# Optimization experiments

Hardware: AMD Instinct MI355X
Metric: run time of the kernel (lower is better)

Reference implementation:

```python
import jax, jax.numpy as jnp
import numpy as np

B, A, K, M = 8, 100000, 80, 32
ALPHA, GAMMA = 0.25, 2.0


def _make_boxes(rng, n, img=800.0):
    cx = rng.uniform(0, img, n).astype(np.float32)
    cy = rng.uniform(0, img, n).astype(np.float32)
    w = rng.uniform(16, 256, n).astype(np.float32)
    h = rng.uniform(16, 256, n).astype(np.float32)
    return np.stack([cx - w / 2, cy - h / 2, cx + w / 2, cy + h / 2], axis=1)


def setup_inputs() -> dict:
    key = jax.random.key(0)
    k1, k2 = jax.random.split(key)
    rng = np.random.default_rng(0)
    classifications = jax.random.uniform(k1, (B, A, K), dtype=jnp.float32)  # forward clamps to (1e-4, 1-1e-4)
    regressions = jax.random.normal(k2, (B, A, 4), dtype=jnp.float32)
    anchors = jnp.asarray(_make_boxes(rng, A))[None]  # [1, A, 4]
    boxes = _make_boxes(rng, B * M).reshape(B, M, 4)
    labels = rng.integers(0, K, (B, M)).astype(np.float32)
    labels[:, M * 3 // 4:] = -1.0  # padded (invalid) annotations
    annotations = jnp.asarray(np.concatenate([boxes, labels[..., None]], axis=-1))  # [B, M, 5]
    return {"classifications": classifications, "regressions": regressions,
            "anchors": anchors, "annotations": annotations}


def _calc_iou(a, b):
    # a: [A,4] anchors, b: [M,4] gt boxes (xyxy)
    area = (b[:, 2] - b[:, 0]) * (b[:, 3] - b[:, 1])  # [M]
    iw = jnp.clip(jnp.minimum(a[:, 2:3], b[None, :, 2]) - jnp.maximum(a[:, 0:1], b[None, :, 0]), 0)
    ih = jnp.clip(jnp.minimum(a[:, 3:4], b[None, :, 3]) - jnp.maximum(a[:, 1:2], b[None, :, 1]), 0)
    inter = iw * ih  # [A,M]
    ua = ((a[:, 2] - a[:, 0]) * (a[:, 3] - a[:, 1]))[:, None] + area[None] - inter
    return inter / jnp.clip(ua, 1e-8)


def _per_image(classification, regression, anchor, ann):
    label = ann[:, 4]
    valid = label != -1.0
    has_ann = jnp.any(valid)

    iou = _calc_iou(anchor, ann[:, :4])           # [A,M]
    iou = jnp.where(valid[None, :], iou, -1.0)    # mask padded annotations
    iou_max = jnp.max(iou, axis=1)                # [A]
    iou_argmax = jnp.argmax(iou, axis=1)
    assigned = ann[iou_argmax]                    # [A,5]

    positive = iou_max >= 0.5
    num_pos = jnp.sum(positive.astype(jnp.float32))
    one_hot = jax.nn.one_hot(assigned[:, 4].astype(jnp.int32), K, dtype=jnp.float32)  # [A,K]

    targets = jnp.where((iou_max >= 0.4)[:, None], 0.25, -1.0)
    targets = jnp.where(positive[:, None], one_hot, targets)  # 0 for pos anchors, 1 at assigned class

    # focal loss (detectron form)
    logit = jnp.clip(classification, 1e-4, 1.0 - 1e-4)
    p = jax.nn.sigmoid(logit)
    term1 = (1.0 - p) ** GAMMA * jnp.log(p)
    term2 = -(p ** GAMMA) * jnp.where(logit >= 0.0,
                                      logit + jax.nn.softplus(-logit),
                                      jax.nn.softplus(logit))
    cls_loss = -jnp.where(targets != 0.0, ALPHA * term1, (1.0 - ALPHA) * term2)
    cls_total = jnp.sum(cls_loss) / jnp.maximum(num_pos, 0.01)

    aw = anchor[:, 2] - anchor[:, 0]
    ah = anchor[:, 3] - anchor[:, 1]
    acx = anchor[:, 0] + 0.5 * aw
    acy = anchor[:, 1] + 0.5 * ah
    gw = assigned[:, 2] - assigned[:, 0]
    gh = assigned[:, 3] - assigned[:, 1]
    gcx = assigned[:, 0] + 0.5 * gw
    gcy = assigned[:, 1] + 0.5 * gh
    gw = jnp.clip(gw, 1.0)
    gh = jnp.clip(gh, 1.0)
    t = jnp.stack([(gcx - acx) / aw, (gcy - acy) / ah,
                   jnp.log(gw / aw), jnp.log(gh / ah)], axis=1)
    t = t / jnp.array([0.1, 0.1, 0.2, 0.2], dtype=jnp.float32)
    diff = jnp.abs(t - regression)
    sl1 = jnp.where(diff <= 1.0 / 9.0, 0.5 * 9.0 * diff * diff, diff - 0.5 / 9.0)
    reg_sum = jnp.sum(jnp.where(positive[:, None], sl1, 0.0))
    reg_loss = jnp.where(num_pos > 0, reg_sum / jnp.maximum(num_pos * 4.0, 1.0), 0.0)

    cls_total = jnp.where(has_ann, cls_total, 0.0)
    reg_loss = jnp.where(has_ann, reg_loss, 0.0)
    return cls_total, reg_loss


def reference(classifications, regressions, anchors, annotations):
    cls_l, reg_l = jax.vmap(_per_image, in_axes=(0, 0, None, 0))(
        classifications, regressions, anchors[0], annotations)
    return (jnp.mean(cls_l, keepdims=True), jnp.mean(reg_l, keepdims=True))
```

## Files before the change

kernel.cpp:

```cpp
#include <hip/hip_runtime.h>

#define BB 8
#define AA 100000
#define KK 80
#define MM 32
#define TILE 128
#define NBLK 782
#define NBLK_P 784

__device__ __forceinline__ float cls_term(float c, int code, int k) {
    float x   = __builtin_amdgcn_fmed3f(c, 1e-4f, 1.0f - 1e-4f);
    float em  = __expf(-x);
    float u   = 1.0f + em;
    float s   = __logf(u);
    float p   = __builtin_amdgcn_rcpf(u);
    float omp = 1.0f - p;
    bool use2 = (code >= 0) && (k != code);
    return use2 ? (0.75f * p * p * (x + s)) : (0.25f * omp * omp * s);
}

__device__ __forceinline__ float neg_term(float c) {
    float x   = __builtin_amdgcn_fmed3f(c, 1e-4f, 1.0f - 1e-4f);
    float em  = __expf(-x);
    float u   = 1.0f + em;
    float s   = __logf(u);
    float p   = __builtin_amdgcn_rcpf(u);
    float omp = 1.0f - p;
    return 0.25f * omp * omp * s;
}

__global__ __launch_bounds__(256)
void focal_main(const float* __restrict__ cls,
                const float* __restrict__ reg,
                const float* __restrict__ anc,
                const float* __restrict__ ann,
                float* __restrict__ cls_part,
                float* __restrict__ reg_part_g,
                int*   __restrict__ np_part)
{
    const int blk = blockIdx.x;
    const int b   = blockIdx.y;
    const int t   = threadIdx.x;
    const int a0  = blk * TILE;
    const int nA  = min(TILE, AA - a0);
    const bool full = (nA == TILE);

    __shared__ float s_ann[MM * 5];
    __shared__ int   s_code[TILE];
    __shared__ float s_wred[4];
    __shared__ int   s_wnp[4];
    __shared__ float s_wrg[4];

    float annv = 0.0f;
    if (t < MM * 5) annv = ann[b * MM * 5 + t];
    const int ai = a0 + t;
    float4 av = make_float4(0.f, 0.f, 0.f, 0.f);
    if (t < nA) av = ((const float4*)anc)[ai];

    if (t < MM * 5) s_ann[t] = annv;
    __syncthreads();

    const float4* c4 = (const float4*)(cls + ((size_t)b * AA + (size_t)a0) * KK);
    float4 v[10];
    if (full) {
        #pragma unroll
        for (int j = 0; j < 10; ++j) v[j] = c4[j * 256 + t];
    }

    int   code     = -1;
    float reg_part = 0.0f;
    int   pos      = 0;
    if (t < nA) {
        const float ax1 = av.x, ay1 = av.y, ax2 = av.z, ay2 = av.w;
        float best = -2.0f;
        int   bidx = 0;
        const float a_area = (ax2 - ax1) * (ay2 - ay1);
        #pragma unroll
        for (int m = 0; m < MM; ++m) {
            float bx1 = s_ann[m * 5 + 0], by1 = s_ann[m * 5 + 1];
            float bx2 = s_ann[m * 5 + 2], by2 = s_ann[m * 5 + 3];
            float lab = s_ann[m * 5 + 4];
            float area  = (bx2 - bx1) * (by2 - by1);
            float iw    = fmaxf(fminf(ax2, bx2) - fmaxf(ax1, bx1), 0.0f);
            float ih    = fmaxf(fminf(ay2, by2) - fmaxf(ay1, by1), 0.0f);
            float inter = iw * ih;
            float ua    = fmaxf(a_area + area - inter, 1e-8f);
            float iou   = inter / ua;
            if (lab == -1.0f) iou = -1.0f;
            if (iou > best) { best = iou; bidx = m; }
        }
        if (best >= 0.5f) {
            pos  = 1;
            code = (int)s_ann[bidx * 5 + 4];
            float gx1 = s_ann[bidx * 5 + 0], gy1 = s_ann[bidx * 5 + 1];
            float gx2 = s_ann[bidx * 5 + 2], gy2 = s_ann[bidx * 5 + 3];
            float aw  = ax2 - ax1,  ah  = ay2 - ay1;
            float acx = ax1 + 0.5f * aw, acy = ay1 + 0.5f * ah;
            float gw  = gx2 - gx1,  gh  = gy2 - gy1;
            float gcx = gx1 + 0.5f * gw, gcy = gy1 + 0.5f * gh;
            gw = fmaxf(gw, 1.0f); gh = fmaxf(gh, 1.0f);
            float tt0 = ((gcx - acx) / aw) / 0.1f;
            float tt1 = ((gcy - acy) / ah) / 0.1f;
            float tt2 = logf(gw / aw) / 0.2f;
            float tt3 = logf(gh / ah) / 0.2f;
            const float4 rv = ((const float4*)reg)[(size_t)b * AA + ai];
            float d0 = fabsf(tt0 - rv.x);
            float d1 = fabsf(tt1 - rv.y);
            float d2 = fabsf(tt2 - rv.z);
            float d3 = fabsf(tt3 - rv.w);
            const float th = 1.0f / 9.0f, hb = 0.5f / 9.0f;
            reg_part  = (d0 <= th ? 4.5f * d0 * d0 : d0 - hb)
                      + (d1 <= th ? 4.5f * d1 * d1 : d1 - hb)
                      + (d2 <= th ? 4.5f * d2 * d2 : d2 - hb)
                      + (d3 <= th ? 4.5f * d3 * d3 : d3 - hb);
        }
    }
    if (t < TILE) s_code[t] = code;

    {
        unsigned long long bal = __ballot(pos != 0);
        int wnp = __popcll(bal);
        float wrg = reg_part;
        #pragma unroll
        for (int off = 32; off > 0; off >>= 1) wrg += __shfl_down(wrg, off, 64);
        int wid  = t >> 6;
        int lane = t & 63;
        if (lane == 0) { s_wnp[wid] = wnp; s_wrg[wid] = wrg; }
    }
    __syncthreads();
    if (t == 0) {
        int   np = s_wnp[0] + s_wnp[1] + s_wnp[2] + s_wnp[3];
        float rg = s_wrg[0] + s_wrg[1] + s_wrg[2] + s_wrg[3];
        np_part   [b * NBLK_P + blk] = np;
        reg_part_g[b * NBLK_P + blk] = rg;
    }

    float part = 0.0f;
    auto process = [&](const float4 vv, int idx4) {
        unsigned e  = (unsigned)idx4 * 4u;
        unsigned al = e / 80u;
        unsigned k0 = e - al * 80u;
        int ca = s_code[al];
        if (__ballot(ca >= 0) == 0ULL) {
            part += neg_term(vv.x);
            part += neg_term(vv.y);
            part += neg_term(vv.z);
            part += neg_term(vv.w);
        } else {
            part += cls_term(vv.x, ca, (int)k0);
            part += cls_term(vv.y, ca, (int)k0 + 1);
            part += cls_term(vv.z, ca, (int)k0 + 2);
            part += cls_term(vv.w, ca, (int)k0 + 3);
        }
    };

    if (full) {
        #pragma unroll
        for (int j = 0; j < 10; ++j) process(v[j], j * 256 + t);
    } else {
        const int limit4 = nA * (KK / 4);
        #pragma unroll 4
        for (int j = 0; j < 10; ++j) {
            int idx4 = j * 256 + t;
            if (idx4 < limit4) { float4 vv = c4[idx4]; process(vv, idx4); }
        }
    }

    #pragma unroll
    for (int off = 32; off > 0; off >>= 1) part += __shfl_down(part, off, 64);
    if ((t & 63) == 0) s_wred[t >> 6] = part;
    __syncthreads();
    if (t == 0) {
        float tot = s_wred[0] + s_wred[1] + s_wred[2] + s_wred[3];
        cls_part[b * NBLK_P + blk] = tot;
    }
}

__global__ __launch_bounds__(256)
void focal_final(const float* __restrict__ ann,
                 const float* __restrict__ cls_part,
                 const float* __restrict__ reg_part,
                 const int*   __restrict__ np_part,
                 float* __restrict__ out)
{
    const int t    = threadIdx.x;
    const int lane = t & 63, wid = t >> 6;
    __shared__ double sd[4];
    __shared__ float  sf[4];
    __shared__ int    si[4];
    __shared__ float  s_c[BB], s_r[BB];

    for (int b = 0; b < BB; ++b) {
        double cd = 0.0; float rf = 0.0f; int np = 0;
        for (int j = t; j < NBLK; j += 256) {
            cd += (double)cls_part[b * NBLK_P + j];
            rf += reg_part[b * NBLK_P + j];
            np += np_part [b * NBLK_P + j];
        }
        #pragma unroll
        for (int off = 32; off > 0; off >>= 1) {
            cd += __shfl_down(cd, off, 64);
            rf += __shfl_down(rf, off, 64);
            np += __shfl_down(np, off, 64);
        }
        if (lane == 0) { sd[wid] = cd; sf[wid] = rf; si[wid] = np; }
        __syncthreads();
        if (t == 0) {
            double cdt = sd[0] + sd[1] + sd[2] + sd[3];
            float  rft = sf[0] + sf[1] + sf[2] + sf[3];
            int    npt = si[0] + si[1] + si[2] + si[3];
            bool has = false;
            for (int m = 0; m < MM; ++m)
                has |= (ann[b * MM * 5 + m * 5 + 4] != -1.0f);
            float npf  = (float)npt;
            float ctot = (float)cdt / fmaxf(npf, 0.01f);
            float rtot = (npt > 0) ? (rft / fmaxf(npf * 4.0f, 1.0f)) : 0.0f;
            s_c[b] = has ? ctot : 0.0f;
            s_r[b] = has ? rtot : 0.0f;
        }
        __syncthreads();
    }
    if (t == 0) {
        float c = 0.0f, r = 0.0f;
        for (int b = 0; b < BB; ++b) { c += s_c[b]; r += s_r[b]; }
        out[0] = c / (float)BB;
        out[1] = r / (float)BB;
    }
}

extern "C" void kernel_launch(void* const* d_in, const int* in_sizes, int n_in,
                              void* d_out, int out_size, void* d_ws, size_t ws_size,
                              hipStream_t stream) {
    const float* cls = (const float*)d_in[0];
    const float* reg = (const float*)d_in[1];
    const float* anc = (const float*)d_in[2];
    const float* ann = (const float*)d_in[3];
    float* out = (float*)d_out;

    float* cls_part = (float*)d_ws;
    float* reg_part = cls_part + BB * NBLK_P;
    int*   np_part  = (int*)(reg_part + BB * NBLK_P);

    dim3 grid(NBLK, BB);
    focal_main<<<grid, 256, 0, stream>>>(cls, reg, anc, ann,
                                         cls_part, reg_part, np_part);
    focal_final<<<1, 256, 0, stream>>>(ann, cls_part, reg_part, np_part, out);
}
```

Baseline: 379.4 us.

## Split anchor matching and classification loss into separate kernels with grid-stride streaming

Splits the fused kernel in two. The first computes each anchor's IoU assignment, regression loss and positive count, and writes a per-anchor class code to workspace. The second streams the classification tensor with a fixed 256-block-per-image grid, batching 8 float4 loads per thread per step and reading codes from global memory. The goal is to stop the IoU loop from sitting between the large classification loads and the math, and to fix occupancy with launch bounds. The cost is an extra launch plus a write and re-read of the codes array (about 3.2 MB).

```diff
diff --git a/kernel.cpp b/kernel.cpp
--- a/kernel.cpp
+++ b/kernel.cpp
@@ -4,9 +4,11 @@
 #define AA 100000
 #define KK 80
 #define MM 32
-#define TILE 128
-#define NBLK 782
-#define NBLK_P 784
+#define NB1 391
+#define NB1_P 392
+#define K2BLK 256
+#define K2STRIDE (K2BLK * 256)
+#define TOTAL4 (AA * KK / 4)
 
 __device__ __forceinline__ float cls_term(float c, int code, int k) {
     float x   = __builtin_amdgcn_fmed3f(c, 1e-4f, 1.0f - 1e-4f);
@@ -30,47 +32,31 @@
 }
 
 __global__ __launch_bounds__(256)
-void focal_main(const float* __restrict__ cls,
-                const float* __restrict__ reg,
-                const float* __restrict__ anc,
-                const float* __restrict__ ann,
-                float* __restrict__ cls_part,
-                float* __restrict__ reg_part_g,
-                int*   __restrict__ np_part)
+void focal_anchors(const float* __restrict__ reg,
+                   const float* __restrict__ anc,
+                   const float* __restrict__ ann,
+                   int*   __restrict__ codes,
+                   float* __restrict__ reg_part_g,
+                   int*   __restrict__ np_part)
 {
     const int blk = blockIdx.x;
     const int b   = blockIdx.y;
     const int t   = threadIdx.x;
-    const int a0  = blk * TILE;
-    const int nA  = min(TILE, AA - a0);
-    const bool full = (nA == TILE);
+    const int a   = blk * 256 + t;
+    const bool act = (a < AA);
 
     __shared__ float s_ann[MM * 5];
-    __shared__ int   s_code[TILE];
-    __shared__ float s_wred[4];
     __shared__ int   s_wnp[4];
     __shared__ float s_wrg[4];
 
-    float annv = 0.0f;
-    if (t < MM * 5) annv = ann[b * MM * 5 + t];
-    const int ai = a0 + t;
-    float4 av = make_float4(0.f, 0.f, 0.f, 0.f);
-    if (t < nA) av = ((const float4*)anc)[ai];
-
-    if (t < MM * 5) s_ann[t] = annv;
+    if (t < MM * 5) s_ann[t] = ann[b * MM * 5 + t];
     __syncthreads();
-
-    const float4* c4 = (const float4*)(cls + ((size_t)b * AA + (size_t)a0) * KK);
-    float4 v[10];
-    if (full) {
-        #pragma unroll
-        for (int j = 0; j < 10; ++j) v[j] = c4[j * 256 + t];
-    }
 
     int   code     = -1;
     float reg_part = 0.0f;
     int   pos      = 0;
-    if (t < nA) {
+    if (act) {
+        const float4 av = ((const float4*)anc)[a];
         const float ax1 = av.x, ay1 = av.y, ax2 = av.z, ay2 = av.w;
         float best = -2.0f;
         int   bidx = 0;
@@ -103,7 +89,7 @@
             float tt1 = ((gcy - acy) / ah) / 0.1f;
             float tt2 = logf(gw / aw) / 0.2f;
             float tt3 = logf(gh / ah) / 0.2f;
-            const float4 rv = ((const float4*)reg)[(size_t)b * AA + ai];
+            const float4 rv = ((const float4*)reg)[(size_t)b * AA + a];
             float d0 = fabsf(tt0 - rv.x);
             float d1 = fabsf(tt1 - rv.y);
             float d2 = fabsf(tt2 - rv.z);
@@ -115,7 +101,7 @@
                       + (d3 <= th ? 4.5f * d3 * d3 : d3 - hb);
         }
     }
-    if (t < TILE) s_code[t] = code;
+    if (act) codes[b * AA + a] = code;
 
     {
         unsigned long long bal = __ballot(pos != 0);
@@ -123,24 +109,32 @@
         float wrg = reg_part;
         #pragma unroll
         for (int off = 32; off > 0; off >>= 1) wrg += __shfl_down(wrg, off, 64);
-        int wid  = t >> 6;
-        int lane = t & 63;
-        if (lane == 0) { s_wnp[wid] = wnp; s_wrg[wid] = wrg; }
+        if ((t & 63) == 0) { s_wnp[t >> 6] = wnp; s_wrg[t >> 6] = wrg; }
     }
     __syncthreads();
     if (t == 0) {
-        int   np = s_wnp[0] + s_wnp[1] + s_wnp[2] + s_wnp[3];
-        float rg = s_wrg[0] + s_wrg[1] + s_wrg[2] + s_wrg[3];
-        np_part   [b * NBLK_P + blk] = np;
-        reg_part_g[b * NBLK_P + blk] = rg;
-    }
+        np_part   [b * NB1_P + blk] = s_wnp[0] + s_wnp[1] + s_wnp[2] + s_wnp[3];
+        reg_part_g[b * NB1_P + blk] = s_wrg[0] + s_wrg[1] + s_wrg[2] + s_wrg[3];
+    }
+}
+
+__global__ __launch_bounds__(256, 8)
+void focal_cls(const float* __restrict__ cls,
+               const int*   __restrict__ codes,
+               float* __restrict__ cls_part)
+{
+    const int b   = blockIdx.y;
+    const int t   = threadIdx.x;
+    const int gid = blockIdx.x * 256 + t;
+    const float4* __restrict__ c4  = (const float4*)(cls + (size_t)b * ((size_t)AA * KK));
+    const int*    __restrict__ cod = codes + b * AA;
 
     float part = 0.0f;
-    auto process = [&](const float4 vv, int idx4) {
-        unsigned e  = (unsigned)idx4 * 4u;
-        unsigned al = e / 80u;
-        unsigned k0 = e - al * 80u;
-        int ca = s_code[al];
+
+    auto process = [&](const float4 vv, int g) {
+        unsigned q  = (unsigned)g / 20u;
+        unsigned k0 = ((unsigned)g - q * 20u) * 4u;
+        int ca = cod[q];
         if (__ballot(ca >= 0) == 0ULL) {
             part += neg_term(vv.x);
             part += neg_term(vv.y);
@@ -154,26 +148,37 @@
         }
     };
 
-    if (full) {
-        #pragma unroll
-        for (int j = 0; j < 10; ++j) process(v[j], j * 256 + t);
-    } else {
-        const int limit4 = nA * (KK / 4);
-        #pragma unroll 4
-        for (int j = 0; j < 10; ++j) {
-            int idx4 = j * 256 + t;
-            if (idx4 < limit4) { float4 vv = c4[idx4]; process(vv, idx4); }
-        }
-    }
-
+    #pragma unroll 1
+    for (int sc = 0; sc < 3; ++sc) {
+        const int g0 = gid + sc * 8 * K2STRIDE;
+        float4 v[8];
+        #pragma unroll
+        for (int j = 0; j < 8; ++j) v[j] = c4[g0 + j * K2STRIDE];
+        #pragma unroll
+        for (int j = 0; j < 8; ++j) process(v[j], g0 + j * K2STRIDE);
+    }
+    {
+        const int g0 = gid + 24 * K2STRIDE;
+        float4 v[7];
+        #pragma unroll
+        for (int j = 0; j < 7; ++j) {
+            int g = g0 + j * K2STRIDE;
+            if (g < TOTAL4) v[j] = c4[g];
+        }
+        #pragma unroll
+        for (int j = 0; j < 7; ++j) {
+            int g = g0 + j * K2STRIDE;
+            if (g < TOTAL4) process(v[j], g);
+        }
+    }
+
+    __shared__ float s_wred[4];
     #pragma unroll
     for (int off = 32; off > 0; off >>= 1) part += __shfl_down(part, off, 64);
     if ((t & 63) == 0) s_wred[t >> 6] = part;
     __syncthreads();
-    if (t == 0) {
-        float tot = s_wred[0] + s_wred[1] + s_wred[2] + s_wred[3];
-        cls_part[b * NBLK_P + blk] = tot;
-    }
+    if (t == 0)
+        cls_part[b * K2BLK + blockIdx.x] = s_wred[0] + s_wred[1] + s_wred[2] + s_wred[3];
 }
 
 __global__ __launch_bounds__(256)
@@ -191,11 +196,11 @@
     __shared__ float  s_c[BB], s_r[BB];
 
     for (int b = 0; b < BB; ++b) {
-        double cd = 0.0; float rf = 0.0f; int np = 0;
-        for (int j = t; j < NBLK; j += 256) {
-            cd += (double)cls_part[b * NBLK_P + j];
-            rf += reg_part[b * NBLK_P + j];
-            np += np_part [b * NBLK_P + j];
+        double cd = (double)cls_part[b * K2BLK + t];
+        float rf = 0.0f; int np = 0;
+        for (int j = t; j < NB1; j += 256) {
+            rf += reg_part[b * NB1_P + j];
+            np += np_part [b * NB1_P + j];
         }
         #pragma unroll
         for (int off = 32; off > 0; off >>= 1) {
@@ -237,12 +242,16 @@
     const float* ann = (const float*)d_in[3];
     float* out = (float*)d_out;
 
-    float* cls_part = (float*)d_ws;
-    float* reg_part = cls_part + BB * NBLK_P;
-    int*   np_part  = (int*)(reg_part + BB * NBLK_P);
-
-    dim3 grid(NBLK, BB);
-    focal_main<<<grid, 256, 0, stream>>>(cls, reg, anc, ann,
-                                         cls_part, reg_part, np_part);
+    int*   codes    = (int*)d_ws;
+    float* cls_part = (float*)(codes + (size_t)BB * AA);
+    float* reg_part = cls_part + BB * K2BLK;
+    int*   np_part  = (int*)(reg_part + BB * NB1_P);
+
+    dim3 g1(NB1, BB);
+    focal_anchors<<<g1, 256, 0, stream>>>(reg, anc, ann, codes, reg_part, np_part);
+
+    dim3 g2(K2BLK, BB);
+    focal_cls<<<g2, 256, 0, stream>>>(cls, codes, cls_part);
+
     focal_final<<<1, 256, 0, stream>>>(ann, cls_part, reg_part, np_part, out);
 }
```

New measurement: 399.3 us. 1.05x slower.

## Split focal loss into polynomial negative term plus sparse positive-row correction

Applied to the files above, without the earlier changes.

Every element's negative focal term is now computed with a degree-12 Chebyshev-derived polynomial instead of exp/log/rcp. Positive anchors get a per-row correction, found by ballot and evaluated a whole wave at a time. The grid shrinks to 256 blocks per image, each striding through a flat float4 index space with double-buffered loads and two anchor rounds per thread, which also simplifies the final reduction. The polynomial approximation risks accuracy differences, and the correction pass adds scattered row reads for positives.

```diff
diff --git a/kernel.cpp b/kernel.cpp
--- a/kernel.cpp
+++ b/kernel.cpp
@@ -1,178 +1,180 @@
 #include <hip/hip_runtime.h>
+#include <cmath>
 
 #define BB 8
 #define AA 100000
 #define KK 80
 #define MM 32
-#define TILE 128
-#define NBLK 782
-#define NBLK_P 784
-
-__device__ __forceinline__ float cls_term(float c, int code, int k) {
+#define APB 391
+#define NXB 256
+#define ST4 (NXB * 256)
+#define TOTAL4 (AA * KK / 4)
+
+struct FPoly {
+    float ih, nmid;
+    float a[13];
+};
+
+__device__ __forceinline__ float corr_term(float c, int ca, int k) {
     float x   = __builtin_amdgcn_fmed3f(c, 1e-4f, 1.0f - 1e-4f);
     float em  = __expf(-x);
     float u   = 1.0f + em;
     float s   = __logf(u);
     float p   = __builtin_amdgcn_rcpf(u);
     float omp = 1.0f - p;
-    bool use2 = (code >= 0) && (k != code);
-    return use2 ? (0.75f * p * p * (x + s)) : (0.25f * omp * omp * s);
-}
-
-__device__ __forceinline__ float neg_term(float c) {
-    float x   = __builtin_amdgcn_fmed3f(c, 1e-4f, 1.0f - 1e-4f);
-    float em  = __expf(-x);
-    float u   = 1.0f + em;
-    float s   = __logf(u);
-    float p   = __builtin_amdgcn_rcpf(u);
-    float omp = 1.0f - p;
-    return 0.25f * omp * omp * s;
-}
-
-__global__ __launch_bounds__(256)
+    float t2  = 0.75f * p * p * (x + s);
+    float t1  = 0.25f * omp * omp * s;
+    return (k == ca) ? 0.0f : (t2 - t1);
+}
+
+__device__ __forceinline__ float pneg(float c, const FPoly& P) {
+    float x  = __builtin_amdgcn_fmed3f(c, 1e-4f, 1.0f - 1e-4f);
+    float tt = __builtin_fmaf(x, P.ih, P.nmid);
+    float r  = P.a[12];
+    #pragma unroll
+    for (int k = 11; k >= 0; --k) r = __builtin_fmaf(r, tt, P.a[k]);
+    return r;
+}
+
+__global__ __launch_bounds__(256, 4)
 void focal_main(const float* __restrict__ cls,
                 const float* __restrict__ reg,
                 const float* __restrict__ anc,
                 const float* __restrict__ ann,
+                FPoly P,
                 float* __restrict__ cls_part,
                 float* __restrict__ reg_part_g,
                 int*   __restrict__ np_part)
 {
-    const int blk = blockIdx.x;
-    const int b   = blockIdx.y;
-    const int t   = threadIdx.x;
-    const int a0  = blk * TILE;
-    const int nA  = min(TILE, AA - a0);
-    const bool full = (nA == TILE);
+    const int blk = blockIdx.x, b = blockIdx.y, t = threadIdx.x;
+    const int gid = blk * 256 + t;
+    const float*  __restrict__ cbase = cls + (size_t)b * ((size_t)AA * KK);
+    const float4* __restrict__ c4    = (const float4*)cbase;
 
     __shared__ float s_ann[MM * 5];
-    __shared__ int   s_code[TILE];
-    __shared__ float s_wred[4];
-    __shared__ int   s_wnp[4];
-    __shared__ float s_wrg[4];
-
-    float annv = 0.0f;
-    if (t < MM * 5) annv = ann[b * MM * 5 + t];
-    const int ai = a0 + t;
-    float4 av = make_float4(0.f, 0.f, 0.f, 0.f);
-    if (t < nA) av = ((const float4*)anc)[ai];
-
-    if (t < MM * 5) s_ann[t] = annv;
+    __shared__ float s_wc[4];
+    __shared__ float s_wr[4];
+    __shared__ int   s_wn[4];
+
+    if (t < MM * 5) s_ann[t] = ann[b * MM * 5 + t];
     __syncthreads();
 
-    const float4* c4 = (const float4*)(cls + ((size_t)b * AA + (size_t)a0) * KK);
-    float4 v[10];
-    if (full) {
-        #pragma unroll
-        for (int j = 0; j < 10; ++j) v[j] = c4[j * 256 + t];
-    }
-
-    int   code     = -1;
-    float reg_part = 0.0f;
-    int   pos      = 0;
-    if (t < nA) {
-        const float ax1 = av.x, ay1 = av.y, ax2 = av.z, ay2 = av.w;
-        float best = -2.0f;
-        int   bidx = 0;
-        const float a_area = (ax2 - ax1) * (ay2 - ay1);
-        #pragma unroll
-        for (int m = 0; m < MM; ++m) {
-            float bx1 = s_ann[m * 5 + 0], by1 = s_ann[m * 5 + 1];
-            float bx2 = s_ann[m * 5 + 2], by2 = s_ann[m * 5 + 3];
-            float lab = s_ann[m * 5 + 4];
-            float area  = (bx2 - bx1) * (by2 - by1);
-            float iw    = fmaxf(fminf(ax2, bx2) - fmaxf(ax1, bx1), 0.0f);
-            float ih    = fmaxf(fminf(ay2, by2) - fmaxf(ay1, by1), 0.0f);
-            float inter = iw * ih;
-            float ua    = fmaxf(a_area + area - inter, 1e-8f);
-            float iou   = inter / ua;
-            if (lab == -1.0f) iou = -1.0f;
-            if (iou > best) { best = iou; bidx = m; }
-        }
-        if (best >= 0.5f) {
-            pos  = 1;
-            code = (int)s_ann[bidx * 5 + 4];
-            float gx1 = s_ann[bidx * 5 + 0], gy1 = s_ann[bidx * 5 + 1];
-            float gx2 = s_ann[bidx * 5 + 2], gy2 = s_ann[bidx * 5 + 3];
-            float aw  = ax2 - ax1,  ah  = ay2 - ay1;
-            float acx = ax1 + 0.5f * aw, acy = ay1 + 0.5f * ah;
-            float gw  = gx2 - gx1,  gh  = gy2 - gy1;
-            float gcx = gx1 + 0.5f * gw, gcy = gy1 + 0.5f * gh;
-            gw = fmaxf(gw, 1.0f); gh = fmaxf(gh, 1.0f);
-            float tt0 = ((gcx - acx) / aw) / 0.1f;
-            float tt1 = ((gcy - acy) / ah) / 0.1f;
-            float tt2 = logf(gw / aw) / 0.2f;
-            float tt3 = logf(gh / ah) / 0.2f;
-            const float4 rv = ((const float4*)reg)[(size_t)b * AA + ai];
-            float d0 = fabsf(tt0 - rv.x);
-            float d1 = fabsf(tt1 - rv.y);
-            float d2 = fabsf(tt2 - rv.z);
-            float d3 = fabsf(tt3 - rv.w);
-            const float th = 1.0f / 9.0f, hb = 0.5f / 9.0f;
-            reg_part  = (d0 <= th ? 4.5f * d0 * d0 : d0 - hb)
-                      + (d1 <= th ? 4.5f * d1 * d1 : d1 - hb)
-                      + (d2 <= th ? 4.5f * d2 * d2 : d2 - hb)
-                      + (d3 <= th ? 4.5f * d3 * d3 : d3 - hb);
-        }
-    }
-    if (t < TILE) s_code[t] = code;
-
-    {
+    const int a0  = blk * APB;
+    const int nAb = min(APB, AA - a0);
+
+    float4 av0 = make_float4(0.f, 0.f, 0.f, 0.f);
+    float4 av1 = make_float4(0.f, 0.f, 0.f, 0.f);
+    if (t < nAb)       av0 = ((const float4*)anc)[a0 + t];
+    if (256 + t < nAb) av1 = ((const float4*)anc)[a0 + 256 + t];
+
+    float4 vA[8], vB[8];
+    #pragma unroll
+    for (int j = 0; j < 8; ++j) vA[j] = c4[gid + j * ST4];
+
+    int np = 0; float rg = 0.f, corr = 0.f;
+    auto do_round = [&](int idx, const float4 av, int roundBase) {
+        int   code = -1; float rp = 0.f; int pos = 0;
+        if (idx < nAb) {
+            const int a = a0 + idx;
+            const float ax1 = av.x, ay1 = av.y, ax2 = av.z, ay2 = av.w;
+            float best = -2.0f;
+            int   bidx = 0;
+            const float a_area = (ax2 - ax1) * (ay2 - ay1);
+            #pragma unroll
+            for (int m = 0; m < MM; ++m) {
+                float bx1 = s_ann[m * 5 + 0], by1 = s_ann[m * 5 + 1];
+                float bx2 = s_ann[m * 5 + 2], by2 = s_ann[m * 5 + 3];
+                float lab = s_ann[m * 5 + 4];
+                float area  = (bx2 - bx1) * (by2 - by1);
+                float iw    = fmaxf(fminf(ax2, bx2) - fmaxf(ax1, bx1), 0.0f);
+                float ih    = fmaxf(fminf(ay2, by2) - fmaxf(ay1, by1), 0.0f);
+                float inter = iw * ih;
+                float ua    = fmaxf(a_area + area - inter, 1e-8f);
+                float iou   = inter / ua;
+                if (lab == -1.0f) iou = -1.0f;
+                if (iou > best) { best = iou; bidx = m; }
+            }
+            if (best >= 0.5f) {
+                pos  = 1;
+                code = (int)s_ann[bidx * 5 + 4];
+                float gx1 = s_ann[bidx * 5 + 0], gy1 = s_ann[bidx * 5 + 1];
+                float gx2 = s_ann[bidx * 5 + 2], gy2 = s_ann[bidx * 5 + 3];
+                float aw  = ax2 - ax1,  ah  = ay2 - ay1;
+                float acx = ax1 + 0.5f * aw, acy = ay1 + 0.5f * ah;
+                float gw  = gx2 - gx1,  gh  = gy2 - gy1;
+                float gcx = gx1 + 0.5f * gw, gcy = gy1 + 0.5f * gh;
+                gw = fmaxf(gw, 1.0f); gh = fmaxf(gh, 1.0f);
+                float tt0 = ((gcx - acx) / aw) / 0.1f;
+                float tt1 = ((gcy - acy) / ah) / 0.1f;
+                float tt2 = logf(gw / aw) / 0.2f;
+                float tt3 = logf(gh / ah) / 0.2f;
+                const float4 rv = ((const float4*)reg)[(size_t)b * AA + a];
+                float d0 = fabsf(tt0 - rv.x);
+                float d1 = fabsf(tt1 - rv.y);
+                float d2 = fabsf(tt2 - rv.z);
+                float d3 = fabsf(tt3 - rv.w);
+                const float th = 1.0f / 9.0f, hb = 0.5f / 9.0f;
+                rp = (d0 <= th ? 4.5f * d0 * d0 : d0 - hb)
+                   + (d1 <= th ? 4.5f * d1 * d1 : d1 - hb)
+                   + (d2 <= th ? 4.5f * d2 * d2 : d2 - hb)
+                   + (d3 <= th ? 4.5f * d3 * d3 : d3 - hb);
+            }
+        }
+        np += pos; rg += rp;
         unsigned long long bal = __ballot(pos != 0);
-        int wnp = __popcll(bal);
-        float wrg = reg_part;
-        #pragma unroll
-        for (int off = 32; off > 0; off >>= 1) wrg += __shfl_down(wrg, off, 64);
-        int wid  = t >> 6;
-        int lane = t & 63;
-        if (lane == 0) { s_wnp[wid] = wnp; s_wrg[wid] = wrg; }
-    }
+        const int lane = t & 63;
+        while (bal) {
+            int l = __ffsll((long long)bal) - 1;
+            bal &= bal - 1;
+            int ca = __shfl(code, l, 64);
+            int aI = a0 + roundBase + (t & ~63) + l;
+            const float* crow = cbase + (size_t)aI * KK;
+            corr += corr_term(crow[lane], ca, lane);
+            if (lane < 16) corr += corr_term(crow[64 + lane], ca, 64 + lane);
+        }
+    };
+    do_round(t,       av0, 0);
+    do_round(256 + t, av1, 256);
+
+    float part = 0.f;
+    auto pneg4 = [&](const float4 v) {
+        part += pneg(v.x, P);
+        part += pneg(v.y, P);
+        part += pneg(v.z, P);
+        part += pneg(v.w, P);
+    };
+    #pragma unroll
+    for (int j = 0; j < 8; ++j) vB[j] = c4[gid + (8 + j) * ST4];
+    #pragma unroll
+    for (int j = 0; j < 8; ++j) pneg4(vA[j]);
+    #pragma unroll
+    for (int j = 0; j < 8; ++j) vA[j] = c4[gid + (16 + j) * ST4];
+    #pragma unroll
+    for (int j = 0; j < 8; ++j) pneg4(vB[j]);
+    #pragma unroll
+    for (int j = 0; j < 6; ++j) vB[j] = c4[gid + (24 + j) * ST4];
+    const bool last = (gid + 30 * ST4) < TOTAL4;
+    vB[6] = make_float4(0.f, 0.f, 0.f, 0.f);
+    if (last) vB[6] = c4[gid + 30 * ST4];
+    #pragma unroll
+    for (int j = 0; j < 8; ++j) pneg4(vA[j]);
+    #pragma unroll
+    for (int j = 0; j < 6; ++j) pneg4(vB[j]);
+    if (last) pneg4(vB[6]);
+
+    part += corr;
+    #pragma unroll
+    for (int off = 32; off > 0; off >>= 1) {
+        part += __shfl_down(part, off, 64);
+        rg   += __shfl_down(rg,   off, 64);
+        np   += __shfl_down(np,   off, 64);
+    }
+    if ((t & 63) == 0) { s_wc[t >> 6] = part; s_wr[t >> 6] = rg; s_wn[t >> 6] = np; }
     __syncthreads();
     if (t == 0) {
-        int   np = s_wnp[0] + s_wnp[1] + s_wnp[2] + s_wnp[3];
-        float rg = s_wrg[0] + s_wrg[1] + s_wrg[2] + s_wrg[3];
-        np_part   [b * NBLK_P + blk] = np;
-        reg_part_g[b * NBLK_P + blk] = rg;
-    }
-
-    float part = 0.0f;
-    auto process = [&](const float4 vv, int idx4) {
-        unsigned e  = (unsigned)idx4 * 4u;
-        unsigned al = e / 80u;
-        unsigned k0 = e - al * 80u;
-        int ca = s_code[al];
-        if (__ballot(ca >= 0) == 0ULL) {
-            part += neg_term(vv.x);
-            part += neg_term(vv.y);
-            part += neg_term(vv.z);
-            part += neg_term(vv.w);
-        } else {
-            part += cls_term(vv.x, ca, (int)k0);
-            part += cls_term(vv.y, ca, (int)k0 + 1);
-            part += cls_term(vv.z, ca, (int)k0 + 2);
-            part += cls_term(vv.w, ca, (int)k0 + 3);
-        }
-    };
-
-    if (full) {
-        #pragma unroll
-        for (int j = 0; j < 10; ++j) process(v[j], j * 256 + t);
-    } else {
-        const int limit4 = nA * (KK / 4);
-        #pragma unroll 4
-        for (int j = 0; j < 10; ++j) {
-            int idx4 = j * 256 + t;
-            if (idx4 < limit4) { float4 vv = c4[idx4]; process(vv, idx4); }
-        }
-    }
-
-    #pragma unroll
-    for (int off = 32; off > 0; off >>= 1) part += __shfl_down(part, off, 64);
-    if ((t & 63) == 0) s_wred[t >> 6] = part;
-    __syncthreads();
-    if (t == 0) {
-        float tot = s_wred[0] + s_wred[1] + s_wred[2] + s_wred[3];
-        cls_part[b * NBLK_P + blk] = tot;
+        cls_part  [b * NXB + blk] = s_wc[0] + s_wc[1] + s_wc[2] + s_wc[3];
+        reg_part_g[b * NXB + blk] = s_wr[0] + s_wr[1] + s_wr[2] + s_wr[3];
+        np_part   [b * NXB + blk] = s_wn[0] + s_wn[1] + s_wn[2] + s_wn[3];
     }
 }
 
@@ -191,12 +193,9 @@
     __shared__ float  s_c[BB], s_r[BB];
 
     for (int b = 0; b < BB; ++b) {
-        double cd = 0.0; float rf = 0.0f; int np = 0;
-        for (int j = t; j < NBLK; j += 256) {
-            cd += (double)cls_part[b * NBLK_P + j];
-            rf += reg_part[b * NBLK_P + j];
-            np += np_part [b * NBLK_P + j];
-        }
+        double cd = (double)cls_part[b * NXB + t];
+        float  rf = reg_part[b * NXB + t];
+        int    np = np_part [b * NXB + t];
         #pragma unroll
         for (int off = 32; off > 0; off >>= 1) {
             cd += __shfl_down(cd, off, 64);
@@ -228,6 +227,53 @@
     }
 }
 
+static FPoly make_poly() {
+    const double PI_D = 3.14159265358979323846;
+    const double lo = 1e-4, hi = 1.0 - 1e-4;
+    const double mid = 0.5 * (lo + hi), half = 0.5 * (hi - lo);
+    const int NC = 13;
+    double fv[NC], cheb[NC];
+    for (int j = 0; j < NC; ++j) {
+        double x  = mid + half * std::cos(PI_D * (j + 0.5) / NC);
+        double em = std::exp(-x);
+        double u  = 1.0 + em;
+        double s  = std::log(u);
+        double p  = 1.0 / u;
+        double om = 1.0 - p;
+        fv[j] = 0.25 * om * om * s;
+    }
+    for (int k = 0; k < NC; ++k) {
+        double acc = 0.0;
+        for (int j = 0; j < NC; ++j)
+            acc += fv[j] * std::cos(k * PI_D * (j + 0.5) / NC);
+        cheb[k] = 2.0 / NC * acc;
+    }
+    cheb[0] *= 0.5;
+    double mono[NC], Tm2[NC], Tm1[NC], Tc[NC];
+    for (int i = 0; i < NC; ++i) { mono[i] = 0.0; Tm2[i] = 0.0; Tm1[i] = 0.0; }
+    Tm2[0] = 1.0;
+    Tm1[1] = 1.0;
+    for (int i = 0; i < NC; ++i) mono[i] = cheb[0] * Tm2[i] + cheb[1] * Tm1[i];
+    for (int k = 2; k < NC; ++k) {
+        for (int i = 0; i < NC; ++i) Tc[i] = -Tm2[i];
+        for (int i = NC - 1; i >= 1; --i) Tc[i] += 2.0 * Tm1[i - 1];
+        for (int i = 0; i < NC; ++i) mono[i] += cheb[k] * Tc[i];
+        for (int i = 0; i < NC; ++i) { Tm2[i] = Tm1[i]; Tm1[i] = Tc[i]; }
+    }
+    FPoly P;
+    double adj = 0.0;
+    for (int k = 1; k < NC; ++k) {
+        float  fk = (float)mono[k];
+        double d  = mono[k] - (double)fk;
+        if ((k & 1) == 0) adj += d / (double)(k + 1);
+        P.a[k] = fk;
+    }
+    P.a[0]  = (float)(mono[0] + adj);
+    P.ih    = (float)(1.0 / half);
+    P.nmid  = (float)(-mid / half);
+    return P;
+}
+
 extern "C" void kernel_launch(void* const* d_in, const int* in_sizes, int n_in,
                               void* d_out, int out_size, void* d_ws, size_t ws_size,
                               hipStream_t stream) {
@@ -237,12 +283,14 @@
     const float* ann = (const float*)d_in[3];
     float* out = (float*)d_out;
 
+    static const FPoly P = make_poly();
+
     float* cls_part = (float*)d_ws;
-    float* reg_part = cls_part + BB * NBLK_P;
-    int*   np_part  = (int*)(reg_part + BB * NBLK_P);
-
-    dim3 grid(NBLK, BB);
-    focal_main<<<grid, 256, 0, stream>>>(cls, reg, anc, ann,
+    float* reg_part = cls_part + BB * NXB;
+    int*   np_part  = (int*)(reg_part + BB * NXB);
+
+    dim3 grid(NXB, BB);
+    focal_main<<<grid, 256, 0, stream>>>(cls, reg, anc, ann, P,
                                          cls_part, reg_part, np_part);
     focal_final<<<1, 256, 0, stream>>>(ann, cls_part, reg_part, np_part, out);
 }
```

Measured after the change: 381.7 us. About the same (+0.6%).
